# Optimization experiments

Hardware: AMD Instinct MI355X
Metric: run time of the kernel (lower is better)

Reference implementation:

```python
import jax, jax.numpy as jnp
import numpy as np

N_NODES = 100000
N_EDGES = 1600000
IN_FEATS = 128
HIDDEN = 128
OUT_DIM = 128


def setup_inputs() -> dict:
    key = jax.random.key(0)
    ks = jax.random.split(key, 8)
    x = jax.random.normal(ks[0], (N_NODES, IN_FEATS), dtype=jnp.float32)
    W1 = jax.random.normal(ks[1], (IN_FEATS, HIDDEN), dtype=jnp.float32) * (1.0 / np.sqrt(IN_FEATS))
    b1 = jnp.zeros((HIDDEN,), dtype=jnp.float32)
    W2 = jax.random.normal(ks[2], (HIDDEN, HIDDEN), dtype=jnp.float32) * (1.0 / np.sqrt(HIDDEN))
    b2 = jnp.zeros((HIDDEN,), dtype=jnp.float32)
    W3 = jax.random.normal(ks[3], (HIDDEN, OUT_DIM), dtype=jnp.float32) * (1.0 / np.sqrt(HIDDEN))
    b3 = jnp.zeros((OUT_DIM,), dtype=jnp.float32)
    edge_src = jax.random.randint(ks[4], (N_EDGES,), 0, N_NODES, dtype=jnp.int32)
    edge_dst = jax.random.randint(ks[5], (N_EDGES,), 0, N_NODES, dtype=jnp.int32)
    return {"x": x, "W1": W1, "b1": b1, "W2": W2, "b2": b2, "W3": W3, "b3": b3,
            "edge_src": edge_src, "edge_dst": edge_dst}


def _mean_agg(h, edge_src, edge_dst, inv_deg):
    # gather src features, scatter-sum to dst, divide by in-degree (mean)
    summed = jax.ops.segment_sum(h[edge_src], edge_dst, num_segments=N_NODES)
    return summed * inv_deg[:, None]


def reference(x, W1, b1, W2, b2, W3, b3, edge_src, edge_dst):
    # in-degree (clamped to 1 to avoid div-by-zero, matching mean over empty = 0)
    deg = jax.ops.segment_sum(jnp.ones((N_EDGES,), dtype=jnp.float32), edge_dst,
                              num_segments=N_NODES)
    inv_deg = 1.0 / jnp.maximum(deg, 1.0)

    # DGL GINConv (eps=0, mean): h = Linear(h + mean_neighbors(h))
    h = x
    h = (h + _mean_agg(h, edge_src, edge_dst, inv_deg)) @ W1 + b1
    h = jax.nn.relu(h)  # dropout inactive in eval mode
    h = (h + _mean_agg(h, edge_src, edge_dst, inv_deg)) @ W2 + b2
    h = jax.nn.relu(h)
    h = (h + _mean_agg(h, edge_src, edge_dst, inv_deg)) @ W3 + b3
    return h
```

## Files before the change

### kernel.cpp

```cpp
#include <hip/hip_runtime.h>
#include <hip/hip_bf16.h>
#include <stdint.h>

#if __has_builtin(__builtin_amdgcn_cvt_pk_f32_fp8) && __has_builtin(__builtin_amdgcn_cvt_pk_fp8_f32)
#define FP8_HW 1
#else
#define FP8_HW 0
#include <hip/hip_fp8.h>
#endif

#define N_NODES 100000
#define N_EDGES 1600000
#define FEAT 128

#define BKT_SHIFT 8
#define BKT_SIZE  256
#define NB_BKT    391
#define BKT_CAP   5664
#define NB_SC     800
#define EPB_SC    2000

#define PREP_CVT 6250
#define PREP_W   192
#define PREP_H   800

typedef uint16_t u16;
typedef uint32_t u32;
typedef __attribute__((ext_vector_type(8))) short bf16x8;
typedef __attribute__((ext_vector_type(4))) float f32x4;
typedef __attribute__((ext_vector_type(2))) float f32x2;

__device__ __forceinline__ u16 bf16_rn(float f){
  u32 u = __float_as_uint(f);
  u += 0x7FFFu + ((u >> 16) & 1u);
  return (u16)(u >> 16);
}
__device__ __forceinline__ float bf16_lo(u32 p){ return __uint_as_float(p << 16); }
__device__ __forceinline__ float bf16_hi(u32 p){ return __uint_as_float(p & 0xFFFF0000u); }

__device__ __forceinline__ void fp8x4_to_f32(u32 w, float* o){
#if FP8_HW
  f32x2 a = __builtin_amdgcn_cvt_pk_f32_fp8(w, false);
  f32x2 b = __builtin_amdgcn_cvt_pk_f32_fp8(w, true);
  o[0] = a.x; o[1] = a.y; o[2] = b.x; o[3] = b.y;
#else
  #pragma unroll
  for (int i = 0; i < 4; ++i){
    __hip_fp8_e4m3 t; t.__x = (uint8_t)((w >> (8 * i)) & 0xFF);
    o[i] = (float)t;
  }
#endif
}
__device__ __forceinline__ u32 f32x4_to_fp8(float a, float b, float c, float d){
#if FP8_HW
  u32 r = __builtin_amdgcn_cvt_pk_fp8_f32(a, b, 0, false);
  r = __builtin_amdgcn_cvt_pk_fp8_f32(c, d, r, true);
  return r;
#else
  __hip_fp8_e4m3 qa(a), qb(b), qc(c), qd(d);
  return (u32)qa.__x | ((u32)qb.__x << 8) | ((u32)qc.__x << 16) | ((u32)qd.__x << 24);
#endif
}

__device__ __forceinline__ void acc_row(uint2 r, f32x2* acc){
#if FP8_HW
  acc[0] += __builtin_amdgcn_cvt_pk_f32_fp8(r.x, false);
  acc[1] += __builtin_amdgcn_cvt_pk_f32_fp8(r.x, true);
  acc[2] += __builtin_amdgcn_cvt_pk_f32_fp8(r.y, false);
  acc[3] += __builtin_amdgcn_cvt_pk_f32_fp8(r.y, true);
#else
  float t0[4], t1[4];
  fp8x4_to_f32(r.x, t0); fp8x4_to_f32(r.y, t1);
  acc[0].x += t0[0]; acc[0].y += t0[1]; acc[1].x += t0[2]; acc[1].y += t0[3];
  acc[2].x += t1[0]; acc[2].y += t1[1]; acc[3].x += t1[2]; acc[3].y += t1[3];
#endif
}


__global__ __launch_bounds__(256) void prep_kernel(
    const float* __restrict__ x,
    const float* __restrict__ W1, const float* __restrict__ W2,
    const float* __restrict__ W3, const int* __restrict__ edst,
    uint2* __restrict__ X8, u16* __restrict__ Wp1, u16* __restrict__ Wp2,
    u16* __restrict__ Wp3, int* __restrict__ hcnt){
  __shared__ int h[NB_BKT];
  int blk = blockIdx.x;
  if (blk < PREP_CVT){
    int i = blk * 256 + threadIdx.x;
    const float4* p = (const float4*)x + (size_t)i * 2;
    float4 a = p[0], b = p[1];
    uint2 o;
    o.x = f32x4_to_fp8(a.x, a.y, a.z, a.w);
    o.y = f32x4_to_fp8(b.x, b.y, b.z, b.w);
    X8[i] = o;
  } else if (blk < PREP_CVT + PREP_W){
    int b = blk - PREP_CVT;
    int which = b >> 6;
    const float* W = (which == 0) ? W1 : (which == 1) ? W2 : W3;
    u16*        Wp = (which == 0) ? Wp1 : (which == 1) ? Wp2 : Wp3;
    int idx = (b & 63) * 256 + threadIdx.x;
    int j    = idx & 7;
    int lane = (idx >> 3) & 63;
    int t    = idx >> 9;
    int k0 = t & 3, n0 = t >> 2;
    int k = k0 * 32 + (lane >> 4) * 8 + j;
    int n = n0 * 16 + (lane & 15);
    Wp[idx] = bf16_rn(W[k * FEAT + n]);
  } else {
    int hb = blk - (PREP_CVT + PREP_W);
    for (int i = threadIdx.x; i < NB_BKT; i += 256) h[i] = 0;
    __syncthreads();
    int base = hb * EPB_SC;
    for (int e = base + threadIdx.x; e < base + EPB_SC; e += 256)
      atomicAdd(&h[edst[e] >> BKT_SHIFT], 1);
    __syncthreads();
    for (int i = threadIdx.x; i < NB_BKT; i += 256)
      hcnt[hb * NB_BKT + i] = h[i];
  }
}


__global__ void hscan_kernel(int* __restrict__ hcnt, int* __restrict__ cursor){
  __shared__ int s[256];
  int b = blockIdx.x, t = threadIdx.x;
  int v[4]; int sum = 0;
  #pragma unroll
  for (int j = 0; j < 4; ++j){
    int blk = 4 * t + j;
    v[j] = (blk < NB_SC) ? hcnt[blk * NB_BKT + b] : 0;
    sum += v[j];
  }
  s[t] = sum;
  __syncthreads();
  for (int d = 1; d < 256; d <<= 1){
    int add = (t >= d) ? s[t - d] : 0;
    __syncthreads();
    s[t] += add;
    __syncthreads();
  }
  int excl = s[t] - sum;
  #pragma unroll
  for (int j = 0; j < 4; ++j){
    int blk = 4 * t + j;
    if (blk < NB_SC){ hcnt[blk * NB_BKT + b] = excl; excl += v[j]; }
  }
  if (t == 255) cursor[b] = s[255];
}

__global__ __launch_bounds__(512) void scatter_kernel(const int* __restrict__ src,
                                                      const int* __restrict__ dst,
                                                      const int* __restrict__ hcnt,
                                                      u32* __restrict__ bbuf){
  __shared__ int cur[NB_BKT];
  for (int i = threadIdx.x; i < NB_BKT; i += 512)
    cur[i] = hcnt[blockIdx.x * NB_BKT + i];
  __syncthreads();
  int base = blockIdx.x * EPB_SC;
  for (int e = base + threadIdx.x; e < base + EPB_SC; e += 512){
    int d = dst[e];
    int b = d >> BKT_SHIFT;
    int p = atomicAdd(&cur[b], 1);
    bbuf[(size_t)b * BKT_CAP + p] = (u32)src[e] | ((u32)(d & (BKT_SIZE - 1)) << 24);
  }
}

__global__ __launch_bounds__(1024) void csr_build_kernel(const u32* __restrict__ bbuf,
                                 const int* __restrict__ cursor,
                                 int* __restrict__ offs, int* __restrict__ deg,
                                 float* __restrict__ inv_deg, int* __restrict__ eidx){
  __shared__ u32 bloc[BKT_CAP];
  __shared__ int seg[BKT_CAP];
  __shared__ int hist[BKT_SIZE];
  __shared__ int s[BKT_SIZE];
  __shared__ int cu[BKT_SIZE];
  __shared__ int stot;
  int b = blockIdx.x;
  int t = threadIdx.x;
  int lo = b * BKT_CAP;
  int n  = cursor[b];
  for (int e = t; e < n; e += 1024) bloc[e] = bbuf[lo + e];
  if (t < BKT_SIZE) hist[t] = 0;
  __syncthreads();
  for (int e = t; e < n; e += 1024)
    atomicAdd(&hist[bloc[e] >> 24], 1);
  __syncthreads();
  int v = 0, pv = 0;
  if (t < BKT_SIZE){
    v  = hist[t];
    pv = (v + 7) & ~7;
    s[t] = pv;
  }
  __syncthreads();
  for (int d = 1; d < BKT_SIZE; d <<= 1){
    int add = (t < BKT_SIZE && t >= d) ? s[t - d] : 0;
    __syncthreads();
    if (t < BKT_SIZE && t >= d) s[t] += add;
    __syncthreads();
  }
  int excl = 0, node = -1;
  if (t < BKT_SIZE){
    excl = s[t] - pv;
    node = b * BKT_SIZE + t;
    if (node < N_NODES){
      offs[node]    = lo + excl;
      deg[node]     = v;
      inv_deg[node] = 1.0f / fmaxf((float)v, 1.0f);
      for (int p = v; p < pv; ++p) seg[excl + p] = 0;
    }
    s[t]  = excl;
    cu[t] = 0;
    if (t == BKT_SIZE - 1) stot = excl + pv;
  }
  __syncthreads();
  for (int e = t; e < n; e += 1024){
    u32 q = bloc[e];
    int y = (int)(q >> 24);
    int p = atomicAdd(&cu[y], 1);
    seg[s[y] + p] = (int)(q & 0xFFFFFFu);
  }
  __syncthreads();
  if (t < BKT_SIZE && node < N_NODES && v > 1){
    for (int i = 1; i < v; ++i){
      int key = seg[excl + i];
      int j = i - 1;
      while (j >= 0 && seg[excl + j] > key){
        seg[excl + j + 1] = seg[excl + j];
        --j;
      }
      seg[excl + j + 1] = key;
    }
  }
  __syncthreads();
  int tot = stot;
  for (int e = t; e < tot; e += 1024) eidx[lo + e] = seg[e];
  if (t < 32 && tot + 32 <= BKT_CAP) eidx[lo + tot + t] = 0;
}


template<int SM, int OUT>
__global__ __launch_bounds__(128, 8) void layer_kernel(
    const u32* __restrict__ n8,
    const u16* __restrict__ hb,
    const float* __restrict__ xf,
    const int* __restrict__ offs,
    const int* __restrict__ deg,
    const float* __restrict__ inv_deg,
    const int* __restrict__ eidx,
    const u16* __restrict__ Wp,
    const float* __restrict__ bias,
    u16* __restrict__ Hout,
    u32* __restrict__ H8out,
    float* __restrict__ Fout){
  __shared__ u16 Tt[16 * FEAT];
  const int tid   = threadIdx.x;
  const int wid   = tid >> 6;
  const int lane  = tid & 63;
  const int nsub  = lane >> 4;
  const int slice = lane & 15;
  const int base  = blockIdx.x * 16;
  const u32* gbase = n8 + slice * 2;

  for (int g = 0; g < 2; ++g){
    const int rrow = wid * 8 + (g << 2) + nsub;
    const int node = base + rrow;
    const int start = offs[node];
    const int cnt   = deg[node];
    const int pcnt  = (cnt + 7) & ~7;
    const int* ep = eidx + start;

    f32x2 acc[4];
    #pragma unroll
    for (int j = 0; j < 4; ++j) acc[j] = (f32x2){0.f, 0.f};

    uint2 rc[8];
    #pragma unroll
    for (int j = 0; j < 8; ++j) rc[j] = make_uint2(0u, 0u);
    if (pcnt > 0){
      uint4 q0 = *(const uint4*)ep;
      uint4 q1 = *(const uint4*)(ep + 4);
      rc[0] = *(const uint2*)(gbase + (size_t)q0.x * 32);
      rc[1] = *(const uint2*)(gbase + (size_t)q0.y * 32);
      rc[2] = *(const uint2*)(gbase + (size_t)q0.z * 32);
      rc[3] = *(const uint2*)(gbase + (size_t)q0.w * 32);
      rc[4] = *(const uint2*)(gbase + (size_t)q1.x * 32);
      rc[5] = *(const uint2*)(gbase + (size_t)q1.y * 32);
      rc[6] = *(const uint2*)(gbase + (size_t)q1.z * 32);
      rc[7] = *(const uint2*)(gbase + (size_t)q1.w * 32);
    }
    uint4 qn1 = *(const uint4*)(ep + 8);
    uint4 qn2 = *(const uint4*)(ep + 12);

    for (int e = 0; e < pcnt; e += 8){
      uint2 rn[8];
      rn[0] = *(const uint2*)(gbase + (size_t)qn1.x * 32);
      rn[1] = *(const uint2*)(gbase + (size_t)qn1.y * 32);
      rn[2] = *(const uint2*)(gbase + (size_t)qn1.z * 32);
      rn[3] = *(const uint2*)(gbase + (size_t)qn1.w * 32);
      rn[4] = *(const uint2*)(gbase + (size_t)qn2.x * 32);
      rn[5] = *(const uint2*)(gbase + (size_t)qn2.y * 32);
      rn[6] = *(const uint2*)(gbase + (size_t)qn2.z * 32);
      rn[7] = *(const uint2*)(gbase + (size_t)qn2.w * 32);
      qn1 = *(const uint4*)(ep + e + 16);
      qn2 = *(const uint4*)(ep + e + 20);
      #pragma unroll
      for (int j = 0; j < 8; ++j) acc_row(rc[j], acc);
      #pragma unroll
      for (int j = 0; j < 8; ++j) rc[j] = rn[j];
    }

    if (pcnt > cnt){
      float f = (float)(pcnt - cnt);
      uint2 rz = *(const uint2*)gbase;
      f32x2 z[4];
      #pragma unroll
      for (int j = 0; j < 4; ++j) z[j] = (f32x2){0.f, 0.f};
      acc_row(rz, z);
      #pragma unroll
      for (int j = 0; j < 4; ++j) acc[j] -= f * z[j];
    }

    const float w = inv_deg[node];
    float self[8];
    if (SM == 1){
      const float* sp = xf + (size_t)node * FEAT + slice * 8;
      float4 a = *(const float4*)sp;
      float4 b = *(const float4*)(sp + 4);
      self[0]=a.x; self[1]=a.y; self[2]=a.z; self[3]=a.w;
      self[4]=b.x; self[5]=b.y; self[6]=b.z; self[7]=b.w;
    } else {
      const u16* sp = hb + (size_t)node * FEAT + slice * 8;
      uint4 s0 = *(const uint4*)sp;
      self[0]=bf16_lo(s0.x); self[1]=bf16_hi(s0.x); self[2]=bf16_lo(s0.y); self[3]=bf16_hi(s0.y);
      self[4]=bf16_lo(s0.z); self[5]=bf16_hi(s0.z); self[6]=bf16_lo(s0.w); self[7]=bf16_hi(s0.w);
    }
    uint4 o;
    o.x = (u32)bf16_rn(self[0] + w*acc[0].x) | ((u32)bf16_rn(self[1] + w*acc[0].y) << 16);
    o.y = (u32)bf16_rn(self[2] + w*acc[1].x) | ((u32)bf16_rn(self[3] + w*acc[1].y) << 16);
    o.z = (u32)bf16_rn(self[4] + w*acc[2].x) | ((u32)bf16_rn(self[5] + w*acc[2].y) << 16);
    o.w = (u32)bf16_rn(self[6] + w*acc[3].x) | ((u32)bf16_rn(self[7] + w*acc[3].y) << 16);
    ((uint4*)Tt)[rrow * 16 + (slice ^ (rrow & 7))] = o;
  }
  __syncthreads();

  const int quad = lane >> 4;
  const int c    = lane & 15;

  bf16x8 A[4];
  #pragma unroll
  for (int k0 = 0; k0 < 4; ++k0){
    uint4 t = ((const uint4*)Tt)[c * 16 + ((quad + k0 * 4) ^ (c & 7))];
    A[k0] = *(const bf16x8*)&t;
  }
  if (OUT == 0) __syncthreads();

  f32x4 acc2[4];
  #pragma unroll
  for (int i = 0; i < 4; ++i) acc2[i] = (f32x4){0.f, 0.f, 0.f, 0.f};
  #pragma unroll
  for (int i = 0; i < 4; ++i){
    int n0 = wid * 4 + i;
    #pragma unroll
    for (int k0 = 0; k0 < 4; ++k0){
      bf16x8 b = *(const bf16x8*)(Wp + (size_t)(((n0 << 2) | k0) * 64 + lane) * 8);
      acc2[i] = __builtin_amdgcn_mfma_f32_16x16x32_bf16(A[k0], b, acc2[i], 0, 0, 0);
    }
  }
  #pragma unroll
  for (int i = 0; i < 4; ++i){
    int n0 = wid * 4 + i;
    float bv = bias[n0 * 16 + c];
    #pragma unroll
    for (int r = 0; r < 4; ++r){
      int rr  = quad * 4 + r;
      int col = n0 * 16 + c;
      if (OUT == 1){
        Fout[(size_t)(base + rr) * FEAT + col] = acc2[i][r] + bv;
      } else {
        float v = fmaxf(acc2[i][r] + bv, 0.f);
        Tt[rr * FEAT + (col ^ ((rr & 7) << 3))] = bf16_rn(v);
      }
    }
  }

  if (OUT == 0){
    __syncthreads();
    #pragma unroll
    for (int it = 0; it < 2; ++it){
      int p  = it * 128 + tid;
      int rr = p >> 4, qq = p & 15;
      int node = base + rr;
      uint4 d = ((const uint4*)Tt)[rr * 16 + (qq ^ (rr & 7))];
      *(uint4*)(Hout + (size_t)node * FEAT + qq * 8) = d;
      uint2 o8;
      o8.x = f32x4_to_fp8(bf16_lo(d.x), bf16_hi(d.x), bf16_lo(d.y), bf16_hi(d.y));
      o8.y = f32x4_to_fp8(bf16_lo(d.z), bf16_hi(d.z), bf16_lo(d.w), bf16_hi(d.w));
      *(uint2*)(H8out + (size_t)node * 32 + qq * 2) = o8;
    }
  }
}


static inline size_t align_up(size_t x){ return (x + 255) & ~(size_t)255; }

extern "C" void kernel_launch(void* const* d_in, const int* in_sizes, int n_in,
                              void* d_out, int out_size, void* d_ws, size_t ws_size,
                              hipStream_t stream){
  const float* x  = (const float*)d_in[0];
  const float* W1 = (const float*)d_in[1];
  const float* b1 = (const float*)d_in[2];
  const float* W2 = (const float*)d_in[3];
  const float* b2 = (const float*)d_in[4];
  const float* W3 = (const float*)d_in[5];
  const float* b3 = (const float*)d_in[6];
  const int* esrc = (const int*)d_in[7];
  const int* edst = (const int*)d_in[8];

  char* w = (char*)d_ws;
  int*   deg     = (int*)w;    w += align_up((size_t)N_NODES * 4);
  int*   offs    = (int*)w;    w += align_up((size_t)N_NODES * 4);
  float* inv_deg = (float*)w;  w += align_up((size_t)N_NODES * 4);
  int*   eidx    = (int*)w;    w += align_up((size_t)NB_BKT * BKT_CAP * 4);
  u16*   Wp1     = (u16*)w;    w += align_up((size_t)16384 * 2);
  u16*   Wp2     = (u16*)w;    w += align_up((size_t)16384 * 2);
  u16*   Wp3     = (u16*)w;    w += align_up((size_t)16384 * 2);
  u16*   Hb      = (u16*)w;    w += align_up((size_t)N_NODES * FEAT * 2);
  u32*   H8b     = (u32*)w;    w += align_up((size_t)N_NODES * 32 * 4);

  u32* bbuf   = (u32*)Hb;
  int* cursor = (int*)H8b;
  int* hcnt   = (int*)((char*)H8b + align_up((size_t)NB_BKT * 4));

  u16* Ha  = (u16*)d_out;
  u32* H8a = (u32*)((char*)d_out + (size_t)N_NODES * FEAT * 2);
  u32* X8  = (u32*)((char*)d_out + (size_t)N_NODES * FEAT * 3);

  prep_kernel<<<PREP_CVT + PREP_W + PREP_H, 256, 0, stream>>>(
      x, W1, W2, W3, edst, (uint2*)X8, Wp1, Wp2, Wp3, hcnt);
  hscan_kernel<<<NB_BKT, 256, 0, stream>>>(hcnt, cursor);
  scatter_kernel<<<NB_SC, 512, 0, stream>>>(esrc, edst, hcnt, bbuf);
  csr_build_kernel<<<NB_BKT, 1024, 0, stream>>>(bbuf, cursor, offs, deg, inv_deg, eidx);

  const int LAYER_BLOCKS = N_NODES / 16;

  layer_kernel<1, 0><<<LAYER_BLOCKS, 128, 0, stream>>>(
      X8, (const u16*)nullptr, x, offs, deg, inv_deg, eidx, Wp1, b1,
      Ha, H8a, (float*)nullptr);

  layer_kernel<0, 0><<<LAYER_BLOCKS, 128, 0, stream>>>(
      H8a, Ha, (const float*)nullptr, offs, deg, inv_deg, eidx, Wp2, b2,
      Hb, H8b, (float*)nullptr);

  layer_kernel<0, 1><<<LAYER_BLOCKS, 128, 0, stream>>>(
      H8b, Hb, (const float*)nullptr, offs, deg, inv_deg, eidx, Wp3, b3,
      (u16*)nullptr, (u32*)nullptr, (float*)d_out);

  (void)in_sizes; (void)n_in; (void)out_size; (void)ws_size; (void)w;
}
```

Before: 334.7 us.

## Replace histogram-scan bucket placement with global atomic cursors and drop neighbor sort

```diff
diff --git a/kernel.cpp b/kernel.cpp
--- a/kernel.cpp
+++ b/kernel.cpp
@@ -22,7 +22,6 @@
 
 #define PREP_CVT 6250
 #define PREP_W   192
-#define PREP_H   800
 
 typedef uint16_t u16;
 typedef uint32_t u32;
@@ -80,10 +79,9 @@
 __global__ __launch_bounds__(256) void prep_kernel(
     const float* __restrict__ x,
     const float* __restrict__ W1, const float* __restrict__ W2,
-    const float* __restrict__ W3, const int* __restrict__ edst,
+    const float* __restrict__ W3,
     uint2* __restrict__ X8, u16* __restrict__ Wp1, u16* __restrict__ Wp2,
-    u16* __restrict__ Wp3, int* __restrict__ hcnt){
-  __shared__ int h[NB_BKT];
+    u16* __restrict__ Wp3, int* __restrict__ gcur){
   int blk = blockIdx.x;
   if (blk < PREP_CVT){
     int i = blk * 256 + threadIdx.x;
@@ -107,60 +105,42 @@
     int n = n0 * 16 + (lane & 15);
     Wp[idx] = bf16_rn(W[k * FEAT + n]);
   } else {
-    int hb = blk - (PREP_CVT + PREP_W);
-    for (int i = threadIdx.x; i < NB_BKT; i += 256) h[i] = 0;
-    __syncthreads();
-    int base = hb * EPB_SC;
-    for (int e = base + threadIdx.x; e < base + EPB_SC; e += 256)
-      atomicAdd(&h[edst[e] >> BKT_SHIFT], 1);
-    __syncthreads();
-    for (int i = threadIdx.x; i < NB_BKT; i += 256)
-      hcnt[hb * NB_BKT + i] = h[i];
-  }
-}
-
-
-__global__ void hscan_kernel(int* __restrict__ hcnt, int* __restrict__ cursor){
-  __shared__ int s[256];
-  int b = blockIdx.x, t = threadIdx.x;
-  int v[4]; int sum = 0;
-  #pragma unroll
-  for (int j = 0; j < 4; ++j){
-    int blk = 4 * t + j;
-    v[j] = (blk < NB_SC) ? hcnt[blk * NB_BKT + b] : 0;
-    sum += v[j];
-  }
-  s[t] = sum;
-  __syncthreads();
-  for (int d = 1; d < 256; d <<= 1){
-    int add = (t >= d) ? s[t - d] : 0;
-    __syncthreads();
-    s[t] += add;
-    __syncthreads();
-  }
-  int excl = s[t] - sum;
-  #pragma unroll
-  for (int j = 0; j < 4; ++j){
-    int blk = 4 * t + j;
-    if (blk < NB_SC){ hcnt[blk * NB_BKT + b] = excl; excl += v[j]; }
-  }
-  if (t == 255) cursor[b] = s[255];
-}
+    for (int i = threadIdx.x; i < NB_BKT; i += 256) gcur[i] = 0;
+  }
+}
+
 
 __global__ __launch_bounds__(512) void scatter_kernel(const int* __restrict__ src,
                                                       const int* __restrict__ dst,
-                                                      const int* __restrict__ hcnt,
+                                                      int* __restrict__ gcur,
                                                       u32* __restrict__ bbuf){
   __shared__ int cur[NB_BKT];
-  for (int i = threadIdx.x; i < NB_BKT; i += 512)
-    cur[i] = hcnt[blockIdx.x * NB_BKT + i];
+  int t = threadIdx.x;
+  for (int i = t; i < NB_BKT; i += 512) cur[i] = 0;
   __syncthreads();
   int base = blockIdx.x * EPB_SC;
-  for (int e = base + threadIdx.x; e < base + EPB_SC; e += 512){
-    int d = dst[e];
-    int b = d >> BKT_SHIFT;
-    int p = atomicAdd(&cur[b], 1);
-    bbuf[(size_t)b * BKT_CAP + p] = (u32)src[e] | ((u32)(d & (BKT_SIZE - 1)) << 24);
+  int dv[4], bv[4];
+  #pragma unroll
+  for (int j = 0; j < 4; ++j){
+    int o = j * 512 + t;
+    dv[j] = (o < EPB_SC) ? dst[base + o] : -1;
+    bv[j] = (dv[j] >= 0) ? (dv[j] >> BKT_SHIFT) : 0;
+    if (dv[j] >= 0) atomicAdd(&cur[bv[j]], 1);
+  }
+  __syncthreads();
+  for (int i = t; i < NB_BKT; i += 512){
+    int c = cur[i];
+    cur[i] = c ? atomicAdd(&gcur[i], c) : 0;
+  }
+  __syncthreads();
+  #pragma unroll
+  for (int j = 0; j < 4; ++j){
+    int o = j * 512 + t;
+    if (dv[j] >= 0){
+      int p = atomicAdd(&cur[bv[j]], 1);
+      bbuf[(size_t)bv[j] * BKT_CAP + p] =
+          (u32)src[base + o] | ((u32)(dv[j] & (BKT_SIZE - 1)) << 24);
+    }
   }
 }
 
@@ -169,7 +149,6 @@
                                  int* __restrict__ offs, int* __restrict__ deg,
                                  float* __restrict__ inv_deg, int* __restrict__ eidx){
   __shared__ u32 bloc[BKT_CAP];
-  __shared__ int seg[BKT_CAP];
   __shared__ int hist[BKT_SIZE];
   __shared__ int s[BKT_SIZE];
   __shared__ int cu[BKT_SIZE];
@@ -197,15 +176,14 @@
     if (t < BKT_SIZE && t >= d) s[t] += add;
     __syncthreads();
   }
-  int excl = 0, node = -1;
   if (t < BKT_SIZE){
-    excl = s[t] - pv;
-    node = b * BKT_SIZE + t;
+    int excl = s[t] - pv;
+    int node = b * BKT_SIZE + t;
     if (node < N_NODES){
       offs[node]    = lo + excl;
       deg[node]     = v;
       inv_deg[node] = 1.0f / fmaxf((float)v, 1.0f);
-      for (int p = v; p < pv; ++p) seg[excl + p] = 0;
+      for (int p = v; p < pv; ++p) eidx[lo + excl + p] = 0;
     }
     s[t]  = excl;
     cu[t] = 0;
@@ -216,23 +194,9 @@
     u32 q = bloc[e];
     int y = (int)(q >> 24);
     int p = atomicAdd(&cu[y], 1);
-    seg[s[y] + p] = (int)(q & 0xFFFFFFu);
-  }
-  __syncthreads();
-  if (t < BKT_SIZE && node < N_NODES && v > 1){
-    for (int i = 1; i < v; ++i){
-      int key = seg[excl + i];
-      int j = i - 1;
-      while (j >= 0 && seg[excl + j] > key){
-        seg[excl + j + 1] = seg[excl + j];
-        --j;
-      }
-      seg[excl + j + 1] = key;
-    }
-  }
-  __syncthreads();
+    eidx[lo + s[y] + p] = (int)(q & 0xFFFFFFu);
+  }
   int tot = stot;
-  for (int e = t; e < tot; e += 1024) eidx[lo + e] = seg[e];
   if (t < 32 && tot + 32 <= BKT_CAP) eidx[lo + tot + t] = 0;
 }
 
@@ -426,19 +390,17 @@
   u16*   Hb      = (u16*)w;    w += align_up((size_t)N_NODES * FEAT * 2);
   u32*   H8b     = (u32*)w;    w += align_up((size_t)N_NODES * 32 * 4);
 
-  u32* bbuf   = (u32*)Hb;
-  int* cursor = (int*)H8b;
-  int* hcnt   = (int*)((char*)H8b + align_up((size_t)NB_BKT * 4));
+  u32* bbuf = (u32*)Hb;
+  int* gcur = (int*)H8b;
 
   u16* Ha  = (u16*)d_out;
   u32* H8a = (u32*)((char*)d_out + (size_t)N_NODES * FEAT * 2);
   u32* X8  = (u32*)((char*)d_out + (size_t)N_NODES * FEAT * 3);
 
-  prep_kernel<<<PREP_CVT + PREP_W + PREP_H, 256, 0, stream>>>(
-      x, W1, W2, W3, edst, (uint2*)X8, Wp1, Wp2, Wp3, hcnt);
-  hscan_kernel<<<NB_BKT, 256, 0, stream>>>(hcnt, cursor);
-  scatter_kernel<<<NB_SC, 512, 0, stream>>>(esrc, edst, hcnt, bbuf);
-  csr_build_kernel<<<NB_BKT, 1024, 0, stream>>>(bbuf, cursor, offs, deg, inv_deg, eidx);
+  prep_kernel<<<PREP_CVT + PREP_W + 1, 256, 0, stream>>>(
+      x, W1, W2, W3, (uint2*)X8, Wp1, Wp2, Wp3, gcur);
+  scatter_kernel<<<NB_SC, 512, 0, stream>>>(esrc, edst, gcur, bbuf);
+  csr_build_kernel<<<NB_BKT, 1024, 0, stream>>>(bbuf, gcur, offs, deg, inv_deg, eidx);
 
   const int LAYER_BLOCKS = N_NODES / 16;
 
```

Measured after the change: 295.4 us. 11.7% less time.
